# Kernel optimization log

Measured on AMD Instinct MI355X. Metric: run time of the kernel, lower is better.

Reference implementation:

```python
import jax, jax.numpy as jnp
import numpy as np

N = 50000        # nodes
E = 800000       # edges (avg degree 16)
F_IN, F_HID, F_OUT = 128, 256, 256
G = 64           # graphs in batch
NEG_SLOPE_ATT = 0.2   # GATConv attention leaky relu
NEG_SLOPE_ACT = 0.01  # nn.LeakyReLU default


def setup_inputs() -> dict:
    key = jax.random.key(0)
    ks = jax.random.split(key, 12)
    x = jax.random.normal(ks[0], (N, F_IN), dtype=jnp.float32)
    edge_index = jax.random.randint(ks[1], (2, E), 0, N, dtype=jnp.int64)
    batch = jnp.sort(jax.random.randint(ks[2], (N,), 0, G, dtype=jnp.int64))
    def glorot(k, shape):
        fan = sum(shape)
        s = jnp.sqrt(6.0 / fan).astype(jnp.float32)
        return jax.random.uniform(k, shape, jnp.float32, -s, s)
    W1 = glorot(ks[3], (F_IN, F_HID))
    a_s1 = glorot(ks[4], (F_HID,))
    a_d1 = glorot(ks[5], (F_HID,))
    b1 = jnp.zeros((F_HID,), jnp.float32)
    W2 = glorot(ks[6], (F_HID, F_OUT))
    a_s2 = glorot(ks[7], (F_OUT,))
    a_d2 = glorot(ks[8], (F_OUT,))
    b2 = jnp.zeros((F_OUT,), jnp.float32)
    return dict(x=x, edge_index=edge_index, batch=batch,
                W1=W1, a_s1=a_s1, a_d1=a_d1, b1=b1,
                W2=W2, a_s2=a_s2, a_d2=a_d2, b2=b2)


def gat_conv(x, src, dst, W, a_s, a_d, b):
    """Single-head PyG GATConv (self-loops already appended to src/dst)."""
    n = x.shape[0]
    h = x @ W                                   # [N, D]
    alpha_src = h @ a_s                         # [N]
    alpha_dst = h @ a_d                         # [N]
    e = jax.nn.leaky_relu(alpha_src[src] + alpha_dst[dst], NEG_SLOPE_ATT)  # [E+N]
    m = jax.ops.segment_max(e, dst, num_segments=n)
    p = jnp.exp(e - jax.lax.stop_gradient(m)[dst])
    denom = jax.ops.segment_sum(p, dst, num_segments=n)
    alpha = p / denom[dst]                      # softmax over incoming edges
    out = jax.ops.segment_sum(h[src] * alpha[:, None], dst, num_segments=n)
    return out + b


def reference(x, edge_index, batch, W1, a_s1, a_d1, b1, W2, a_s2, a_d2, b2):
    n = x.shape[0]
    loops = jnp.arange(n, dtype=edge_index.dtype)   # GATConv add_self_loops=True
    src = jnp.concatenate([edge_index[0], loops])
    dst = jnp.concatenate([edge_index[1], loops])
    h = gat_conv(x, src, dst, W1, a_s1, a_d1, b1)
    h = jax.nn.leaky_relu(h, NEG_SLOPE_ACT)         # dropout is identity in eval
    node_emb = gat_conv(h, src, dst, W2, a_s2, a_d2, b2)
    graph_emb = jax.ops.segment_sum(node_emb, batch, num_segments=G)
    return node_emb, graph_emb
```

## Files before the change

### kernel.cpp

```cpp
#include <hip/hip_runtime.h>
#include <math.h>

#define NN 50000
#define NE 800000
#define F_IN 128
#define F_HID 256
#define NG 64
#define NPART 8
#define CSR_CHUNKS 128
#define SLOTS 64

typedef __bf16 bf16x8 __attribute__((ext_vector_type(8)));
typedef float f32x4 __attribute__((ext_vector_type(4)));
typedef float f32x2 __attribute__((ext_vector_type(2)));
typedef unsigned short u16x8 __attribute__((ext_vector_type(8)));

static __device__ __forceinline__ unsigned short f2bf(float f) {
    union { float f; unsigned u; } v; v.f = f;
    unsigned r = v.u + 0x7fff + ((v.u >> 16) & 1);
    return (unsigned short)(r >> 16);
}
static __device__ __forceinline__ float bf2f(unsigned short u) {
    union { unsigned u; float f; } v; v.u = ((unsigned)u) << 16;
    return v.f;
}
static __device__ __forceinline__ f32x2 bf2x2(unsigned u) {
    union { unsigned u; float f; } lo, hi;
    lo.u = u << 16;
    hi.u = u & 0xffff0000u;
    f32x2 r; r[0] = lo.f; r[1] = hi.f;
    return r;
}

template <int K, bool AF32>
__global__ __launch_bounds__(256)
void gemm_mfma(const void* __restrict__ Ap, const ushort* __restrict__ Wt,
               ushort* __restrict__ C16, const float* __restrict__ a_s,
               const float* __restrict__ a_d, float* __restrict__ as_out,
               float* __restrict__ ad_out, int M) {
    const ushort* A16 = (const ushort*)Ap;
    const float* A32 = (const float*)Ap;
    __shared__ ushort As[128 * 40];
    __shared__ ushort Bs[128 * 40];
    const int t = threadIdx.x;
    const int bm = blockIdx.x * 128, bn = blockIdx.y * 128;
    const int wv = t >> 6, lane = t & 63;
    const int wm = (wv & 1) * 64, wn = (wv >> 1) * 64;
    const int lrow = lane & 15, quad = lane >> 4;
    const int srow = t >> 2;
    const int skp = (t & 3) << 3;

    f32x4 acc[4][4];
    #pragma unroll
    for (int i = 0; i < 4; ++i)
        #pragma unroll
        for (int j = 0; j < 4; ++j)
            #pragma unroll
            for (int r = 0; r < 4; ++r) acc[i][j][r] = 0.f;

    const int r0 = bm + srow, r1 = bm + srow + 64;
    const int rb0 = bn + srow, rb1 = bn + srow + 64;

    auto load_a = [&](int k0, u16x8& a0, u16x8& a1) {
        a0 = (u16x8)(0); a1 = (u16x8)(0);
        if (AF32) {
            if (r0 < M) {
                const float* p = A32 + (size_t)r0 * K + k0 + skp;
                float4 f0 = *(const float4*)p, f1 = *(const float4*)(p + 4);
                a0[0]=f2bf(f0.x); a0[1]=f2bf(f0.y); a0[2]=f2bf(f0.z); a0[3]=f2bf(f0.w);
                a0[4]=f2bf(f1.x); a0[5]=f2bf(f1.y); a0[6]=f2bf(f1.z); a0[7]=f2bf(f1.w);
            }
            if (r1 < M) {
                const float* p = A32 + (size_t)r1 * K + k0 + skp;
                float4 f0 = *(const float4*)p, f1 = *(const float4*)(p + 4);
                a1[0]=f2bf(f0.x); a1[1]=f2bf(f0.y); a1[2]=f2bf(f0.z); a1[3]=f2bf(f0.w);
                a1[4]=f2bf(f1.x); a1[5]=f2bf(f1.y); a1[6]=f2bf(f1.z); a1[7]=f2bf(f1.w);
            }
        } else {
            if (r0 < M) a0 = *(const u16x8*)(A16 + (size_t)r0 * K + k0 + skp);
            if (r1 < M) a1 = *(const u16x8*)(A16 + (size_t)r1 * K + k0 + skp);
        }
    };

    u16x8 a0, a1, b0, b1;
    load_a(0, a0, a1);
    b0 = *(const u16x8*)(Wt + (size_t)rb0 * K + skp);
    b1 = *(const u16x8*)(Wt + (size_t)rb1 * K + skp);

    for (int k0 = 0; k0 < K; k0 += 32) {
        __syncthreads();
        *(u16x8*)(As + srow * 40 + skp) = a0;
        *(u16x8*)(As + (srow + 64) * 40 + skp) = a1;
        *(u16x8*)(Bs + srow * 40 + skp) = b0;
        *(u16x8*)(Bs + (srow + 64) * 40 + skp) = b1;
        __syncthreads();
        bool more = (k0 + 32) < K;
        u16x8 na0, na1, nb0, nb1;
        if (more) {
            load_a(k0 + 32, na0, na1);
            nb0 = *(const u16x8*)(Wt + (size_t)rb0 * K + k0 + 32 + skp);
            nb1 = *(const u16x8*)(Wt + (size_t)rb1 * K + k0 + 32 + skp);
        }
        bf16x8 af[4], bf_[4];
        #pragma unroll
        for (int i = 0; i < 4; ++i)
            af[i] = *(const bf16x8*)(As + (wm + i * 16 + lrow) * 40 + quad * 8);
        #pragma unroll
        for (int j = 0; j < 4; ++j)
            bf_[j] = *(const bf16x8*)(Bs + (wn + j * 16 + lrow) * 40 + quad * 8);
        #pragma unroll
        for (int i = 0; i < 4; ++i)
            #pragma unroll
            for (int j = 0; j < 4; ++j)
                acc[i][j] = __builtin_amdgcn_mfma_f32_16x16x32_bf16(
                    af[i], bf_[j], acc[i][j], 0, 0, 0);
        if (more) { a0 = na0; a1 = na1; b0 = nb0; b1 = nb1; }
    }
    float asf[4], adf[4];
    #pragma unroll
    for (int j = 0; j < 4; ++j) {
        asf[j] = a_s[bn + wn + j * 16 + lrow];
        adf[j] = a_d[bn + wn + j * 16 + lrow];
    }
    #pragma unroll
    for (int i = 0; i < 4; ++i) {
        int gm0 = bm + wm + i * 16 + quad * 4;
        #pragma unroll
        for (int r = 0; r < 4; ++r) {
            float ps = 0.f, pd = 0.f;
            #pragma unroll
            for (int j = 0; j < 4; ++j) {
                ps += acc[i][j][r] * asf[j];
                pd += acc[i][j][r] * adf[j];
            }
            #pragma unroll
            for (int off = 8; off; off >>= 1) {
                ps += __shfl_xor(ps, off);
                pd += __shfl_xor(pd, off);
            }
            if (lrow == 0 && gm0 + r < M) {
                atomicAdd(&as_out[gm0 + r], ps);
                atomicAdd(&ad_out[gm0 + r], pd);
            }
        }
        #pragma unroll
        for (int j = 0; j < 4; ++j) {
            int gn = bn + wn + j * 16 + lrow;
            #pragma unroll
            for (int r = 0; r < 4; ++r)
                if (gm0 + r < M) C16[(size_t)(gm0 + r) * 256 + gn] = f2bf(acc[i][j][r]);
        }
    }
}

__global__ void cvt_wts(const float* __restrict__ W1, ushort* __restrict__ Wt1,
                        const float* __restrict__ W2, ushort* __restrict__ Wt2) {
    int idx = blockIdx.x * blockDim.x + threadIdx.x;
    if (idx < 256 * F_IN) {
        int n = idx / F_IN, k = idx - n * F_IN;
        Wt1[idx] = f2bf(W1[(size_t)k * 256 + n]);
    } else if (idx < 256 * F_IN + 256 * F_HID) {
        int i2 = idx - 256 * F_IN;
        int n = i2 / F_HID, k = i2 - n * F_HID;
        Wt2[i2] = f2bf(W2[(size_t)k * 256 + n]);
    }
}

__global__ __launch_bounds__(256)
void scatter_part(const int* __restrict__ src, const int* __restrict__ dst,
                  int* __restrict__ cursor, int* __restrict__ src_sorted,
                  int E, int n) {
    const int p = blockIdx.x & (NPART - 1);
    const int c = blockIdx.x >> 3;
    const int T = E + n;
    const int chunk = (T + CSR_CHUNKS - 1) / CSR_CHUNKS;
    const int i0 = c * chunk;
    const int i1 = min(i0 + chunk, T);
    for (int i = i0 + (int)threadIdx.x; i < i1; i += 256) {
        int d = (i < E) ? dst[i] : (i - E);
        int pd = (d * NPART) / NN;
        if (pd == p) {
            int s = (i < E) ? src[i] : d;
            int pos = atomicAdd(&cursor[d], 1);
            if (pos < SLOTS) src_sorted[(size_t)d * SLOTS + pos] = s;
        }
    }
}

template <bool ACT, bool BF16OUT, bool POOL>
__global__ __launch_bounds__(256)
void agg_kernel(const ushort* __restrict__ h, const float* __restrict__ as,
                const float* __restrict__ ad, const int* __restrict__ degs,
                const int* __restrict__ src_sorted, const float* __restrict__ bias,
                float* __restrict__ out, ushort* __restrict__ out16,
                const int* __restrict__ batch, float* __restrict__ gemb, int n) {
    const int hw = threadIdx.x >> 5;
    const int lane = threadIdx.x & 63;
    const int hl = lane & 31;
    const int base = lane & 32;
    const int node = blockIdx.x * 8 + hw;
    __shared__ float vbuf[8][256];
    __shared__ int gids[8];

    const bool valid = node < n;
    int deg = 0, start = 0;
    float adn = 0.f;
    if (valid) {
        deg = min(degs[node], SLOTS);
        start = node * SLOTS;
        adn = ad[node];
    }

    int s_lane = 0;
    float e_lane = -INFINITY;
    if (valid && hl < deg) {
        s_lane = src_sorted[start + hl];
        float e = as[s_lane] + adn;
        e_lane = e > 0.f ? e : 0.2f * e;
    }
    float m = e_lane;
    for (int j = 32 + hl; j < deg; j += 32) {
        int s = src_sorted[start + j];
        float e = as[s] + adn;
        e = e > 0.f ? e : 0.2f * e;
        m = fmaxf(m, e);
    }
    #pragma unroll
    for (int off = 16; off; off >>= 1) m = fmaxf(m, __shfl_xor(m, off));
    float p_lane = __expf(e_lane - m);
    float denom = p_lane;
    for (int j = 32 + hl; j < deg; j += 32) {
        int s = src_sorted[start + j];
        float e = as[s] + adn;
        e = e > 0.f ? e : 0.2f * e;
        denom += __expf(e - m);
    }
    #pragma unroll
    for (int off = 16; off; off >>= 1) denom += __shfl_xor(denom, off);
    float inv = valid ? (1.f / denom) : 0.f;
    p_lane *= inv;

    const ushort* hrow = h + hl * 8;
    f32x2 acc2[4];
    #pragma unroll
    for (int q = 0; q < 4; ++q) { acc2[q][0] = 0.f; acc2[q][1] = 0.f; }
    const int degc = min(deg, 32);
    for (int j0 = 0; j0 < degc; j0 += 4) {
        float wa = __shfl(p_lane, base | j0);       int sa = __shfl(s_lane, base | j0);
        float wb = __shfl(p_lane, base | (j0 + 1)); int sb = __shfl(s_lane, base | (j0 + 1));
        float wc = __shfl(p_lane, base | (j0 + 2)); int sc = __shfl(s_lane, base | (j0 + 2));
        float wd = __shfl(p_lane, base | (j0 + 3)); int sd = __shfl(s_lane, base | (j0 + 3));
        wb = (j0 + 1 < degc) ? wb : 0.f;
        wc = (j0 + 2 < degc) ? wc : 0.f;
        wd = (j0 + 3 < degc) ? wd : 0.f;
        uint4 ra = *(const uint4*)(hrow + (size_t)sa * 256);
        uint4 rb = *(const uint4*)(hrow + (size_t)sb * 256);
        uint4 rc = *(const uint4*)(hrow + (size_t)sc * 256);
        uint4 rd = *(const uint4*)(hrow + (size_t)sd * 256);
        f32x2 wa2; wa2[0] = wa; wa2[1] = wa;
        f32x2 wb2; wb2[0] = wb; wb2[1] = wb;
        f32x2 wc2; wc2[0] = wc; wc2[1] = wc;
        f32x2 wd2; wd2[0] = wd; wd2[1] = wd;
        acc2[0] += wa2 * bf2x2(ra.x); acc2[1] += wa2 * bf2x2(ra.y);
        acc2[2] += wa2 * bf2x2(ra.z); acc2[3] += wa2 * bf2x2(ra.w);
        acc2[0] += wb2 * bf2x2(rb.x); acc2[1] += wb2 * bf2x2(rb.y);
        acc2[2] += wb2 * bf2x2(rb.z); acc2[3] += wb2 * bf2x2(rb.w);
        acc2[0] += wc2 * bf2x2(rc.x); acc2[1] += wc2 * bf2x2(rc.y);
        acc2[2] += wc2 * bf2x2(rc.z); acc2[3] += wc2 * bf2x2(rc.w);
        acc2[0] += wd2 * bf2x2(rd.x); acc2[1] += wd2 * bf2x2(rd.y);
        acc2[2] += wd2 * bf2x2(rd.z); acc2[3] += wd2 * bf2x2(rd.w);
    }
    if (deg > 32) {
        for (int j = 32; j < deg; ++j) {
            int s = src_sorted[start + j];
            float e = as[s] + adn;
            e = e > 0.f ? e : 0.2f * e;
            float w = __expf(e - m) * inv;
            uint4 r = *(const uint4*)(hrow + (size_t)s * 256);
            f32x2 w2; w2[0] = w; w2[1] = w;
            acc2[0] += w2 * bf2x2(r.x); acc2[1] += w2 * bf2x2(r.y);
            acc2[2] += w2 * bf2x2(r.z); acc2[3] += w2 * bf2x2(r.w);
        }
    }
    const float4* b4 = (const float4*)bias;
    float4 b0 = b4[hl * 2], b1 = b4[hl * 2 + 1];
    float v[8];
    v[0] = acc2[0][0] + b0.x; v[1] = acc2[0][1] + b0.y;
    v[2] = acc2[1][0] + b0.z; v[3] = acc2[1][1] + b0.w;
    v[4] = acc2[2][0] + b1.x; v[5] = acc2[2][1] + b1.y;
    v[6] = acc2[3][0] + b1.z; v[7] = acc2[3][1] + b1.w;
    if (ACT) {
        #pragma unroll
        for (int k = 0; k < 8; ++k) v[k] = v[k] > 0.f ? v[k] : 0.01f * v[k];
    }
    if (valid) {
        if (BF16OUT) {
            u16x8 o;
            #pragma unroll
            for (int k = 0; k < 8; ++k) o[k] = f2bf(v[k]);
            *(u16x8*)(out16 + (size_t)node * 256 + hl * 8) = o;
        } else {
            float4 o0 = make_float4(v[0], v[1], v[2], v[3]);
            float4 o1 = make_float4(v[4], v[5], v[6], v[7]);
            float4* op = (float4*)(out + (size_t)node * 256);
            op[hl * 2] = o0;
            op[hl * 2 + 1] = o1;
        }
    }
    if (POOL) {
        *(float4*)&vbuf[hw][hl * 8]     = make_float4(v[0], v[1], v[2], v[3]);
        *(float4*)&vbuf[hw][hl * 8 + 4] = make_float4(v[4], v[5], v[6], v[7]);
        if (hl == 0) gids[hw] = valid ? batch[node] : -1;
        __syncthreads();
        const int t = threadIdx.x;
        float acc = 0.f;
        int cur = gids[0];
        #pragma unroll
        for (int i = 0; i < 8; ++i) {
            int g = gids[i];
            if (g < 0) break;
            if (g != cur) {
                atomicAdd(&gemb[(size_t)cur * 256 + t], acc);
                acc = 0.f; cur = g;
            }
            acc += vbuf[i][t];
        }
        if (cur >= 0) atomicAdd(&gemb[(size_t)cur * 256 + t], acc);
    }
}

static inline char* align_up(char* p, size_t a) {
    return (char*)(((uintptr_t)p + a - 1) & ~(uintptr_t)(a - 1));
}

extern "C" void kernel_launch(void* const* d_in, const int* in_sizes, int n_in,
                              void* d_out, int out_size, void* d_ws, size_t ws_size,
                              hipStream_t stream) {
    const float* x     = (const float*)d_in[0];
    const int* eidx    = (const int*)d_in[1];
    const int* batch   = (const int*)d_in[2];
    const float* W1    = (const float*)d_in[3];
    const float* a_s1  = (const float*)d_in[4];
    const float* a_d1  = (const float*)d_in[5];
    const float* b1    = (const float*)d_in[6];
    const float* W2    = (const float*)d_in[7];
    const float* a_s2  = (const float*)d_in[8];
    const float* a_d2  = (const float*)d_in[9];
    const float* b2    = (const float*)d_in[10];

    float* node_emb  = (float*)d_out;
    float* graph_emb = node_emb + (size_t)NN * 256;

    char* ws = (char*)d_ws;
    ushort* h16  = (ushort*)ws;  ws += (size_t)NN * 256 * sizeof(ushort);
    ws = align_up(ws, 256);
    ushort* z16  = (ushort*)ws;  ws += (size_t)NN * 256 * sizeof(ushort);
    ws = align_up(ws, 256);
    ushort* wt1  = (ushort*)ws;  ws += (size_t)256 * F_IN * sizeof(ushort);
    ws = align_up(ws, 256);
    ushort* wt2  = (ushort*)ws;  ws += (size_t)256 * F_HID * sizeof(ushort);
    ws = align_up(ws, 256);
    float* as_buf = (float*)ws;  ws += (size_t)NN * sizeof(float);
    float* ad_buf = (float*)ws;  ws += (size_t)NN * sizeof(float);
    int* cursor   = (int*)ws;    ws += (size_t)NN * sizeof(int);
    ws = align_up(ws, 256);
    int* src_sorted = (int*)ws;  ws += (size_t)NN * SLOTS * sizeof(int);

    const int* e_src = eidx;
    const int* e_dst = eidx + NE;

    dim3 gemm_grid((NN + 127) / 128, 2);
    int agg_blocks = (NN + 7) / 8;

    hipMemsetAsync(cursor, 0, (size_t)NN * sizeof(int), stream);
    scatter_part<<<NPART * CSR_CHUNKS, 256, 0, stream>>>(e_src, e_dst, cursor, src_sorted, NE, NN);

    cvt_wts<<<(256 * (F_IN + F_HID) + 255) / 256, 256, 0, stream>>>(W1, wt1, W2, wt2);

    hipMemsetAsync(as_buf, 0, (size_t)2 * NN * sizeof(float), stream);
    gemm_mfma<F_IN, true><<<gemm_grid, 256, 0, stream>>>(x, wt1, h16, a_s1, a_d1, as_buf, ad_buf, NN);
    agg_kernel<true, true, false><<<agg_blocks, 256, 0, stream>>>(
        h16, as_buf, ad_buf, cursor, src_sorted, b1, nullptr, z16, nullptr, nullptr, NN);

    hipMemsetAsync(as_buf, 0, (size_t)2 * NN * sizeof(float), stream);
    hipMemsetAsync(graph_emb, 0, (size_t)NG * 256 * sizeof(float), stream);
    gemm_mfma<F_HID, false><<<gemm_grid, 256, 0, stream>>>(z16, wt2, h16, a_s2, a_d2, as_buf, ad_buf, NN);
    agg_kernel<false, false, true><<<agg_blocks, 256, 0, stream>>>(
        h16, as_buf, ad_buf, cursor, src_sorted, b2, node_emb, nullptr, batch, graph_emb, NN);
}
```

Measured before the change: 318.9 us.

## Use 64x256 GEMM tiles so attention dot products reduce in-block without atomics

The GEMM tile changes from 128x128 on a 2D grid to 64 rows by the full 256 output columns, with each of the four waves owning a 64-column slice. Because a block now covers every output column of its rows, the attention-score dot products are reduced in shared memory and written with plain stores. This removes the float atomics and the two memsets that zeroed the score buffers. In exchange each block reloads the whole weight matrix per K step and runs with fewer rows per block, which may lower A-operand reuse.

Result: faster. 310.4 us (-2.7%).

```diff
diff --git a/kernel.cpp b/kernel.cpp
--- a/kernel.cpp
+++ b/kernel.cpp
@@ -40,12 +40,14 @@
                float* __restrict__ ad_out, int M) {
     const ushort* A16 = (const ushort*)Ap;
     const float* A32 = (const float*)Ap;
-    __shared__ ushort As[128 * 40];
-    __shared__ ushort Bs[128 * 40];
+    __shared__ ushort As[64 * 40];
+    __shared__ ushort Bs[256 * 40];
+    __shared__ float dps[4][64];
+    __shared__ float dpd[4][64];
     const int t = threadIdx.x;
-    const int bm = blockIdx.x * 128, bn = blockIdx.y * 128;
+    const int bm = blockIdx.x * 64;
     const int wv = t >> 6, lane = t & 63;
-    const int wm = (wv & 1) * 64, wn = (wv >> 1) * 64;
+    const int wn = wv * 64;
     const int lrow = lane & 15, quad = lane >> 4;
     const int srow = t >> 2;
     const int skp = (t & 3) << 3;
@@ -58,53 +60,50 @@
             #pragma unroll
             for (int r = 0; r < 4; ++r) acc[i][j][r] = 0.f;
 
-    const int r0 = bm + srow, r1 = bm + srow + 64;
-    const int rb0 = bn + srow, rb1 = bn + srow + 64;
-
-    auto load_a = [&](int k0, u16x8& a0, u16x8& a1) {
-        a0 = (u16x8)(0); a1 = (u16x8)(0);
-        if (AF32) {
-            if (r0 < M) {
+    const int r0 = bm + srow;
+
+    auto load_a = [&](int k0, u16x8& a0) {
+        a0 = (u16x8)(0);
+        if (r0 < M) {
+            if (AF32) {
                 const float* p = A32 + (size_t)r0 * K + k0 + skp;
                 float4 f0 = *(const float4*)p, f1 = *(const float4*)(p + 4);
                 a0[0]=f2bf(f0.x); a0[1]=f2bf(f0.y); a0[2]=f2bf(f0.z); a0[3]=f2bf(f0.w);
                 a0[4]=f2bf(f1.x); a0[5]=f2bf(f1.y); a0[6]=f2bf(f1.z); a0[7]=f2bf(f1.w);
-            }
-            if (r1 < M) {
-                const float* p = A32 + (size_t)r1 * K + k0 + skp;
-                float4 f0 = *(const float4*)p, f1 = *(const float4*)(p + 4);
-                a1[0]=f2bf(f0.x); a1[1]=f2bf(f0.y); a1[2]=f2bf(f0.z); a1[3]=f2bf(f0.w);
-                a1[4]=f2bf(f1.x); a1[5]=f2bf(f1.y); a1[6]=f2bf(f1.z); a1[7]=f2bf(f1.w);
-            }
-        } else {
-            if (r0 < M) a0 = *(const u16x8*)(A16 + (size_t)r0 * K + k0 + skp);
-            if (r1 < M) a1 = *(const u16x8*)(A16 + (size_t)r1 * K + k0 + skp);
+            } else {
+                a0 = *(const u16x8*)(A16 + (size_t)r0 * K + k0 + skp);
+            }
         }
     };
-
-    u16x8 a0, a1, b0, b1;
-    load_a(0, a0, a1);
-    b0 = *(const u16x8*)(Wt + (size_t)rb0 * K + skp);
-    b1 = *(const u16x8*)(Wt + (size_t)rb1 * K + skp);
+    auto load_b = [&](int k0, u16x8& b0, u16x8& b1, u16x8& b2, u16x8& b3) {
+        b0 = *(const u16x8*)(Wt + (size_t)srow * K + k0 + skp);
+        b1 = *(const u16x8*)(Wt + (size_t)(srow + 64) * K + k0 + skp);
+        b2 = *(const u16x8*)(Wt + (size_t)(srow + 128) * K + k0 + skp);
+        b3 = *(const u16x8*)(Wt + (size_t)(srow + 192) * K + k0 + skp);
+    };
+
+    u16x8 a0, b0, b1, b2, b3;
+    load_a(0, a0);
+    load_b(0, b0, b1, b2, b3);
 
     for (int k0 = 0; k0 < K; k0 += 32) {
         __syncthreads();
         *(u16x8*)(As + srow * 40 + skp) = a0;
-        *(u16x8*)(As + (srow + 64) * 40 + skp) = a1;
         *(u16x8*)(Bs + srow * 40 + skp) = b0;
         *(u16x8*)(Bs + (srow + 64) * 40 + skp) = b1;
+        *(u16x8*)(Bs + (srow + 128) * 40 + skp) = b2;
+        *(u16x8*)(Bs + (srow + 192) * 40 + skp) = b3;
         __syncthreads();
         bool more = (k0 + 32) < K;
-        u16x8 na0, na1, nb0, nb1;
+        u16x8 na0, nb0, nb1, nb2, nb3;
         if (more) {
-            load_a(k0 + 32, na0, na1);
-            nb0 = *(const u16x8*)(Wt + (size_t)rb0 * K + k0 + 32 + skp);
-            nb1 = *(const u16x8*)(Wt + (size_t)rb1 * K + k0 + 32 + skp);
+            load_a(k0 + 32, na0);
+            load_b(k0 + 32, nb0, nb1, nb2, nb3);
         }
         bf16x8 af[4], bf_[4];
         #pragma unroll
         for (int i = 0; i < 4; ++i)
-            af[i] = *(const bf16x8*)(As + (wm + i * 16 + lrow) * 40 + quad * 8);
+            af[i] = *(const bf16x8*)(As + (i * 16 + lrow) * 40 + quad * 8);
         #pragma unroll
         for (int j = 0; j < 4; ++j)
             bf_[j] = *(const bf16x8*)(Bs + (wn + j * 16 + lrow) * 40 + quad * 8);
@@ -114,17 +113,16 @@
             for (int j = 0; j < 4; ++j)
                 acc[i][j] = __builtin_amdgcn_mfma_f32_16x16x32_bf16(
                     af[i], bf_[j], acc[i][j], 0, 0, 0);
-        if (more) { a0 = na0; a1 = na1; b0 = nb0; b1 = nb1; }
+        if (more) { a0 = na0; b0 = nb0; b1 = nb1; b2 = nb2; b3 = nb3; }
     }
     float asf[4], adf[4];
     #pragma unroll
     for (int j = 0; j < 4; ++j) {
-        asf[j] = a_s[bn + wn + j * 16 + lrow];
-        adf[j] = a_d[bn + wn + j * 16 + lrow];
+        asf[j] = a_s[wn + j * 16 + lrow];
+        adf[j] = a_d[wn + j * 16 + lrow];
     }
     #pragma unroll
     for (int i = 0; i < 4; ++i) {
-        int gm0 = bm + wm + i * 16 + quad * 4;
         #pragma unroll
         for (int r = 0; r < 4; ++r) {
             float ps = 0.f, pd = 0.f;
@@ -138,14 +136,23 @@
                 ps += __shfl_xor(ps, off);
                 pd += __shfl_xor(pd, off);
             }
-            if (lrow == 0 && gm0 + r < M) {
-                atomicAdd(&as_out[gm0 + r], ps);
-                atomicAdd(&ad_out[gm0 + r], pd);
-            }
-        }
+            if (lrow == 0) {
+                dps[wv][i * 16 + quad * 4 + r] = ps;
+                dpd[wv][i * 16 + quad * 4 + r] = pd;
+            }
+        }
+    }
+    __syncthreads();
+    if (t < 64 && bm + t < M) {
+        as_out[bm + t] = dps[0][t] + dps[1][t] + dps[2][t] + dps[3][t];
+        ad_out[bm + t] = dpd[0][t] + dpd[1][t] + dpd[2][t] + dpd[3][t];
+    }
+    #pragma unroll
+    for (int i = 0; i < 4; ++i) {
+        int gm0 = bm + i * 16 + quad * 4;
         #pragma unroll
         for (int j = 0; j < 4; ++j) {
-            int gn = bn + wn + j * 16 + lrow;
+            int gn = wn + j * 16 + lrow;
             #pragma unroll
             for (int r = 0; r < 4; ++r)
                 if (gm0 + r < M) C16[(size_t)(gm0 + r) * 256 + gn] = f2bf(acc[i][j][r]);
@@ -369,7 +376,7 @@
     const int* e_src = eidx;
     const int* e_dst = eidx + NE;
 
-    dim3 gemm_grid((NN + 127) / 128, 2);
+    int gemm_blocks = (NN + 63) / 64;
     int agg_blocks = (NN + 7) / 8;
 
     hipMemsetAsync(cursor, 0, (size_t)NN * sizeof(int), stream);
@@ -377,14 +384,12 @@
 
     cvt_wts<<<(256 * (F_IN + F_HID) + 255) / 256, 256, 0, stream>>>(W1, wt1, W2, wt2);
 
-    hipMemsetAsync(as_buf, 0, (size_t)2 * NN * sizeof(float), stream);
-    gemm_mfma<F_IN, true><<<gemm_grid, 256, 0, stream>>>(x, wt1, h16, a_s1, a_d1, as_buf, ad_buf, NN);
+    gemm_mfma<F_IN, true><<<gemm_blocks, 256, 0, stream>>>(x, wt1, h16, a_s1, a_d1, as_buf, ad_buf, NN);
     agg_kernel<true, true, false><<<agg_blocks, 256, 0, stream>>>(
         h16, as_buf, ad_buf, cursor, src_sorted, b1, nullptr, z16, nullptr, nullptr, NN);
 
-    hipMemsetAsync(as_buf, 0, (size_t)2 * NN * sizeof(float), stream);
     hipMemsetAsync(graph_emb, 0, (size_t)NG * 256 * sizeof(float), stream);
-    gemm_mfma<F_HID, false><<<gemm_grid, 256, 0, stream>>>(z16, wt2, h16, a_s2, a_d2, as_buf, ad_buf, NN);
+    gemm_mfma<F_HID, false><<<gemm_blocks, 256, 0, stream>>>(z16, wt2, h16, a_s2, a_d2, as_buf, ad_buf, NN);
     agg_kernel<false, false, true><<<agg_blocks, 256, 0, stream>>>(
         h16, as_buf, ad_buf, cursor, src_sorted, b2, node_emb, nullptr, batch, graph_emb, NN);
 }
```
